# Optimization experiments

Hardware: AMD Instinct MI355X
Metric: run time of the kernel (lower is better)

Reference implementation:

```python
import jax, jax.numpy as jnp
import numpy as np

B, N, D_MODEL, H = 2, 2048, 1024, 16
HD = D_MODEL // H  # head_dim = 64

def setup_inputs() -> dict:
    key = jax.random.key(0)
    ks = jax.random.split(key, 5)
    x = jax.random.normal(ks[0], (B, N, D_MODEL), dtype=jnp.float32)
    scale = 0.02
    # Linear weights stored as [in, out] (torch does x @ W.T with W [out,in]; equivalent math)
    Wq = jax.random.normal(ks[1], (D_MODEL, D_MODEL), dtype=jnp.float32) * scale
    Wk = jax.random.normal(ks[2], (D_MODEL, D_MODEL), dtype=jnp.float32) * scale
    Wv = jax.random.normal(ks[3], (D_MODEL, D_MODEL), dtype=jnp.float32) * scale
    Wo = jax.random.normal(ks[4], (D_MODEL, D_MODEL), dtype=jnp.float32) * scale
    return {"x": x, "Wq": Wq, "Wk": Wk, "Wv": Wv, "Wo": Wo}

def reference(x, Wq, Wk, Wv, Wo):
    b, n, _ = x.shape
    # QKV projections (no bias; qkv_bias=False)
    q = (x @ Wq).reshape(b, n, H, HD)
    k = (x @ Wk).reshape(b, n, H, HD)
    v = (x @ Wv).reshape(b, n, H, HD)
    # scores [b, h, q, k]
    scores = jnp.einsum('bqhd,bkhd->bhqk', q, k) / jnp.sqrt(jnp.float32(HD))
    causal = jnp.triu(jnp.ones((n, n), dtype=bool), k=1)  # True above diagonal -> masked
    scores = jnp.where(causal, -jnp.inf, scores)
    attn = jax.nn.softmax(scores, axis=-1)  # dropout p=0.0 -> identity
    ctx = jnp.einsum('bhqk,bkhd->bqhd', attn, v).reshape(b, n, D_MODEL)
    return ctx @ Wo
```

## Files before the change

### kernel.cpp

```cpp
#include <hip/hip_runtime.h>
#include <math.h>

#define D_MODEL 1024
#define NHEAD 16
#define HD 64
#define SEQ 2048
#define BATCH 2
#define MTOT (BATCH * SEQ)

typedef __attribute__((ext_vector_type(8))) short bf16x8;
typedef __attribute__((ext_vector_type(4))) float f32x4;

__device__ __forceinline__ unsigned short f2bf(float f) {
    unsigned int u = __float_as_uint(f);
    u += 0x7FFF + ((u >> 16) & 1);
    return (unsigned short)(u >> 16);
}

__device__ __forceinline__ unsigned int pk2bf(float a, float b) {
    unsigned int r;
    asm("v_cvt_pk_bf16_f32 %0, %1, %2" : "=v"(r) : "v"(a), "v"(b));
    return r;
}

__device__ __forceinline__ void async16(unsigned short* lds, const unsigned short* g) {
    __builtin_amdgcn_global_load_lds(
        (const __attribute__((address_space(1))) unsigned int*)g,
        (__attribute__((address_space(3))) unsigned int*)lds, 16, 0, 0);
}

__device__ __forceinline__ void BAR() {
    asm volatile("" ::: "memory");
    __builtin_amdgcn_s_barrier();
    asm volatile("" ::: "memory");
}

__global__ __launch_bounds__(256) void prep(const float* __restrict__ x,
                                            unsigned short* __restrict__ xb,
                                            const float* __restrict__ W0,
                                            const float* __restrict__ W1,
                                            const float* __restrict__ W2,
                                            const float* __restrict__ W3,
                                            unsigned short* __restrict__ Wt) {
    const int bid = blockIdx.x;
    const int tid = threadIdx.x;
    if (bid < 4096) {
        const int i = (bid * 256 + tid) * 4;
        float4 v = *(const float4*)(x + i);
        uint2 pk;
        pk.x = pk2bf(v.x, v.y);
        pk.y = pk2bf(v.z, v.w);
        *(uint2*)(xb + i) = pk;
    } else {
        __shared__ float T[32][33];
        const int t = bid - 4096;
        const int z = t >> 10, rem = t & 1023;
        const int n0 = (rem & 31) * 32, k0 = (rem >> 5) * 32;
        const float* W = (z == 0) ? W0 : (z == 1) ? W1 : (z == 2) ? W2 : W3;
        unsigned short* out = Wt + (size_t)z * D_MODEL * D_MODEL;
        const int tx = tid & 31, ty = tid >> 5;
#pragma unroll
        for (int i = 0; i < 4; ++i)
            T[ty + 8 * i][tx] = W[(size_t)(k0 + ty + 8 * i) * D_MODEL + n0 + tx];
        __syncthreads();
#pragma unroll
        for (int i = 0; i < 4; ++i)
            out[(size_t)(n0 + ty + 8 * i) * D_MODEL + k0 + tx] = f2bf(T[tx][ty + 8 * i]);
    }
}

__global__ __launch_bounds__(512, 2) void qkv_mfma(const unsigned short* __restrict__ A,
                                                   const unsigned short* __restrict__ Wt,
                                                   unsigned short* __restrict__ q,
                                                   unsigned short* __restrict__ k,
                                                   unsigned short* __restrict__ vt) {
    __shared__ unsigned short SM[40960];
    const int tid = threadIdx.x;
    const int wave = tid >> 6, lane = tid & 63;
    const int quad = lane >> 4, l16 = lane & 15;
    const int wm = wave >> 2, wn = wave & 3;

    const int bid = blockIdx.x;
    const int swz = (bid & 7) * 64 + (bid >> 3);
    const int by = swz >> 4, bx = swz & 15;
    const int m0 = by * 128;
    const int c0 = bx * 192;
    const unsigned short* Bz = Wt;

    const unsigned short* aptr;
    {
        const int s = tid, r = s >> 2;
        const int cg = (s & 3) ^ ((r + (r >> 2)) & 3);
        aptr = A + (size_t)(m0 + r) * D_MODEL + cg * 8;
    }
    const unsigned short* bptr[2];
#pragma unroll
    for (int j = 0; j < 2; ++j) {
        const int s = j * 512 + tid;
        const int r = s >> 2;
        const int cg = (s & 3) ^ ((r + (r >> 2)) & 3);
        const int rb = (r < 192) ? r : 191;
        bptr[j] = Bz + (size_t)(c0 + rb) * D_MODEL + cg * 8;
    }
    const int ldsA0 = wave * 512;
    const int ldsB0 = wave * 512, ldsB1 = 4096 + wave * 512;

    const int key = (l16 + (l16 >> 2)) & 3;
    const int chunk = quad ^ key;
    int aoff[4], boff[3];
#pragma unroll
    for (int mt = 0; mt < 4; ++mt)
        aoff[mt] = ((wm * 64 + mt * 16 + l16) * 4 + chunk) * 8;
#pragma unroll
    for (int nt = 0; nt < 3; ++nt)
        boff[nt] = ((wn * 48 + nt * 16 + l16) * 4 + chunk) * 8;

    f32x4 acc[4][3];
#pragma unroll
    for (int mt = 0; mt < 4; ++mt)
#pragma unroll
        for (int nt = 0; nt < 3; ++nt)
            acc[mt][nt] = (f32x4){0.f, 0.f, 0.f, 0.f};

    auto stageA = [&](int d, int ks, int T) {
        const int base = d * 20480 + ks * 4096;
        async16(SM + base + ldsA0, aptr + T * 64 + ks * 32);
    };
    auto stageB = [&](int d, int ks, int T) {
        const int base = d * 20480 + 8192 + ks * 6144;
        async16(SM + base + ldsB0, bptr[0] + T * 64 + ks * 32);
        if (wave < 4)
            async16(SM + base + ldsB1, bptr[1] + T * 64 + ks * 32);
    };
    auto dsA = [&](bf16x8* af, int mh, int d, int ks) {
        const int base = d * 20480 + ks * 4096;
#pragma unroll
        for (int i = 0; i < 2; ++i)
            af[i] = *(const bf16x8*)&SM[base + aoff[mh * 2 + i]];
    };
    auto dsB = [&](bf16x8* bf, int d, int ks) {
        const int base = d * 20480 + 8192 + ks * 6144;
#pragma unroll
        for (int i = 0; i < 3; ++i)
            bf[i] = *(const bf16x8*)&SM[base + boff[i]];
    };
    auto mfma6 = [&](bf16x8* af, bf16x8* bf, int mh) {
        __builtin_amdgcn_s_setprio(1);
#pragma unroll
        for (int i = 0; i < 2; ++i)
#pragma unroll
            for (int nt = 0; nt < 3; ++nt)
                acc[mh * 2 + i][nt] = __builtin_amdgcn_mfma_f32_16x16x32_bf16(
                    af[i], bf[nt], acc[mh * 2 + i][nt], 0, 0, 0);
        __builtin_amdgcn_s_setprio(0);
    };
    auto waitc = [&](bool nx) {
        if (nx) {
            if (wave < 4) asm volatile("s_waitcnt vmcnt(3)" ::: "memory");
            else          asm volatile("s_waitcnt vmcnt(2)" ::: "memory");
        } else {
            asm volatile("s_waitcnt vmcnt(0)" ::: "memory");
        }
    };

    stageA(0, 0, 0);
    stageB(0, 0, 0);
    stageA(0, 1, 0);
    stageB(0, 1, 0);
    waitc(true);
    BAR();

    const int NT = D_MODEL / 64;
    for (int T = 0; T < NT; ++T) {
        const int d = T & 1, dn = d ^ 1;
        const bool nx = (T + 1 < NT);
        bf16x8 af[2], bf[3];
        dsA(af, 0, d, 0);
        dsB(bf, d, 0);
        if (nx) stageA(dn, 0, T + 1);
        __builtin_amdgcn_sched_barrier(0);
        BAR();
        mfma6(af, bf, 0);
        BAR();
        dsA(af, 1, d, 0);
        if (nx) stageB(dn, 0, T + 1);
        waitc(nx);
        __builtin_amdgcn_sched_barrier(0);
        BAR();
        mfma6(af, bf, 1);
        BAR();
        dsA(af, 0, d, 1);
        dsB(bf, d, 1);
        if (nx) stageA(dn, 1, T + 1);
        __builtin_amdgcn_sched_barrier(0);
        BAR();
        mfma6(af, bf, 0);
        BAR();
        dsA(af, 1, d, 1);
        if (nx) stageB(dn, 1, T + 1);
        waitc(nx);
        __builtin_amdgcn_sched_barrier(0);
        BAR();
        mfma6(af, bf, 1);
        BAR();
    }

    __syncthreads();
    const int bb = m0 >> 11, tok0 = m0 & (SEQ - 1);
#pragma unroll 1
    for (int G = 0; G < 3; ++G) {
        if (G) __syncthreads();
        const int gcol = c0 + G * 64;
        const int zg = gcol >> 10;
        const int hg = (gcol >> 6) & 15;
        if (zg < 2) {
            const float sc = (zg == 0) ? 0.18033688011112042f : 1.0f;
            unsigned short* dst = (zg == 0) ? q : k;
#pragma unroll
            for (int nt = 0; nt < 3; ++nt) {
                const int colb = wn * 48 + nt * 16;
                if ((colb >> 6) == G) {
                    const int cl = colb - G * 64 + l16;
#pragma unroll
                    for (int mt = 0; mt < 4; ++mt)
#pragma unroll
                        for (int reg = 0; reg < 4; ++reg) {
                            const int rr = wm * 64 + mt * 16 + quad * 4 + reg;
                            SM[rr * 64 + cl] = f2bf(acc[mt][nt][reg] * sc);
                        }
                }
            }
            __syncthreads();
#pragma unroll
            for (int it = 0; it < 2; ++it) {
                const int g = it * 512 + tid;
                const int r = g >> 3, c8 = g & 7;
                uint4 val = *(const uint4*)&SM[r * 64 + c8 * 8];
                *(uint4*)(dst + (((size_t)bb * NHEAD + hg) * SEQ + tok0 + r) * HD +
                          c8 * 8) = val;
            }
        } else {
#pragma unroll
            for (int nt = 0; nt < 3; ++nt) {
                const int colb = wn * 48 + nt * 16;
                if ((colb >> 6) == G) {
                    const int dl = colb - G * 64 + l16;
#pragma unroll
                    for (int mt = 0; mt < 4; ++mt) {
                        const int m = wm * 64 + mt * 16 + quad * 4;
                        uint2 w;
                        w.x = pk2bf(acc[mt][nt][0], acc[mt][nt][1]);
                        w.y = pk2bf(acc[mt][nt][2], acc[mt][nt][3]);
                        *(uint2*)&SM[dl * 136 + m] = w;
                    }
                }
            }
            __syncthreads();
#pragma unroll
            for (int it = 0; it < 2; ++it) {
                const int g = it * 512 + tid;
                const int dd = g >> 4, t8 = (g & 15) * 8;
                uint4 val = *(const uint4*)&SM[dd * 136 + t8];
                *(uint4*)(vt + (((size_t)bb * NHEAD + hg) * HD + dd) * SEQ + tok0 +
                          t8) = val;
            }
        }
    }
}

__global__ __launch_bounds__(256) void gemm_out(const unsigned short* __restrict__ A,
                                                const unsigned short* __restrict__ Bw,
                                                float* __restrict__ outf) {
    __shared__ unsigned short SM[12288];
    const int tid = threadIdx.x;
    const int m0 = blockIdx.y * 64, n0 = blockIdx.x * 128;
    const int wave = tid >> 6, lane = tid & 63;
    const int quad = lane >> 4, l16 = lane & 15;
    const int wm = wave & 1, wn = wave >> 1;

    f32x4 acc[2][4];
#pragma unroll
    for (int mt = 0; mt < 2; ++mt)
#pragma unroll
        for (int nt = 0; nt < 4; ++nt)
            acc[mt][nt] = (f32x4){0.f, 0.f, 0.f, 0.f};

    for (int k0 = 0; k0 < D_MODEL; k0 += 64) {
        __syncthreads();
#pragma unroll
        for (int i = 0; i < 2; ++i) {
            const int c = i * 256 + tid;
            const int r = c >> 3, cc = (c & 7) * 8;
            const int cbase = i * 256 + wave * 64;
            async16(SM + cbase * 8, A + (size_t)(m0 + r) * D_MODEL + k0 + cc);
        }
#pragma unroll
        for (int i = 0; i < 4; ++i) {
            const int c = i * 256 + tid;
            const int r = c >> 3, cc = (c & 7) * 8;
            const int cbase = i * 256 + wave * 64;
            async16(SM + 4096 + cbase * 8, Bw + (size_t)(n0 + r) * D_MODEL + k0 + cc);
        }
        __syncthreads();
#pragma unroll
        for (int ks = 0; ks < 2; ++ks) {
            bf16x8 af[2], bfr[4];
#pragma unroll
            for (int mt = 0; mt < 2; ++mt)
                af[mt] = *(const bf16x8*)&SM[(wm * 32 + mt * 16 + l16) * 64 + ks * 32 + quad * 8];
#pragma unroll
            for (int nt = 0; nt < 4; ++nt)
                bfr[nt] = *(const bf16x8*)&SM[4096 + (wn * 64 + nt * 16 + l16) * 64 + ks * 32 + quad * 8];
#pragma unroll
            for (int mt = 0; mt < 2; ++mt)
#pragma unroll
                for (int nt = 0; nt < 4; ++nt)
                    acc[mt][nt] = __builtin_amdgcn_mfma_f32_16x16x32_bf16(
                        af[mt], bfr[nt], acc[mt][nt], 0, 0, 0);
        }
    }

#pragma unroll
    for (int mt = 0; mt < 2; ++mt)
#pragma unroll
        for (int nt = 0; nt < 4; ++nt)
#pragma unroll
            for (int reg = 0; reg < 4; ++reg) {
                const int m = m0 + wm * 32 + mt * 16 + quad * 4 + reg;
                const int n = n0 + wn * 64 + nt * 16 + l16;
                outf[(size_t)m * D_MODEL + n] = acc[mt][nt][reg];
            }
}

__global__ __launch_bounds__(256, 2) void attn_mfma(const unsigned short* __restrict__ Q,
                                                    const unsigned short* __restrict__ K,
                                                    const unsigned short* __restrict__ VT,
                                                    unsigned short* __restrict__ ctx) {
    __shared__ float CMB[8832];
    const int tid = threadIdx.x;
    const int wave = tid >> 6, lane = tid & 63;
    const int quad = lane >> 4, l16 = lane & 15;
    const int h = blockIdx.x, b = blockIdx.z;
    const int y = blockIdx.y;
    const unsigned short* Qp = Q + ((size_t)b * NHEAD + h) * SEQ * HD;
    const unsigned short* Kp = K + ((size_t)b * NHEAD + h) * SEQ * HD;
    const unsigned short* Vp = VT + ((size_t)b * NHEAD + h) * HD * SEQ;
    unsigned short* Pw = (unsigned short*)CMB + wave * 4096;
    const int sw8 = l16 & 7;

#pragma unroll 1
    for (int half = 0; half < 2; ++half) {
        const int p = half ? y : (31 - y);
        const int row0 = p * 64;
        if (half) __syncthreads();

        bf16x8 bQ[4][2];
#pragma unroll
        for (int f = 0; f < 4; ++f)
#pragma unroll
            for (int ks = 0; ks < 2; ++ks)
                bQ[f][ks] = *(const bf16x8*)(Qp +
                    (size_t)(row0 + f * 16 + l16) * HD + ks * 32 + quad * 8);

        f32x4 o[4][4];
        float ps[4] = {0.f, 0.f, 0.f, 0.f};
#pragma unroll
        for (int nt = 0; nt < 4; ++nt)
#pragma unroll
            for (int f = 0; f < 4; ++f)
                o[nt][f] = (f32x4){0.f, 0.f, 0.f, 0.f};

        for (int kt = wave; kt <= p; kt += 4) {
            bf16x8 aK[4][2];
#pragma unroll
            for (int mt = 0; mt < 4; ++mt)
#pragma unroll
                for (int ks = 0; ks < 2; ++ks)
                    aK[mt][ks] = *(const bf16x8*)(Kp +
                        (size_t)(kt * 64 + mt * 16 + l16) * HD + ks * 32 + quad * 8);

            f32x4 sT[4][4];
            __builtin_amdgcn_s_setprio(1);
#pragma unroll
            for (int mt = 0; mt < 4; ++mt)
#pragma unroll
                for (int f = 0; f < 4; ++f) {
                    sT[mt][f] = __builtin_amdgcn_mfma_f32_16x16x32_bf16(
                        aK[mt][0], bQ[f][0], (f32x4){0.f, 0.f, 0.f, 0.f}, 0, 0, 0);
                    sT[mt][f] = __builtin_amdgcn_mfma_f32_16x16x32_bf16(
                        aK[mt][1], bQ[f][1], sT[mt][f], 0, 0, 0);
                }
            __builtin_amdgcn_s_setprio(0);

            bf16x8 aV[4][2];
#pragma unroll
            for (int nt = 0; nt < 4; ++nt)
#pragma unroll
                for (int ks = 0; ks < 2; ++ks)
                    aV[nt][ks] = *(const bf16x8*)(Vp +
                        (size_t)(nt * 16 + l16) * SEQ + kt * 64 + ks * 32 + quad * 8);

            const bool diag = (kt == p);
#pragma unroll
            for (int mt = 0; mt < 4; ++mt)
#pragma unroll
                for (int f = 0; f < 4; ++f) {
                    float pv[4];
#pragma unroll
                    for (int reg = 0; reg < 4; ++reg)
                        pv[reg] = __builtin_amdgcn_exp2f(sT[mt][f][reg]);
                    if (diag) {
                        const int kb = kt * 64 + mt * 16 + quad * 4;
                        const int qg = row0 + f * 16 + l16;
#pragma unroll
                        for (int reg = 0; reg < 4; ++reg)
                            pv[reg] = (kb + reg > qg) ? 0.f : pv[reg];
                    }
                    ps[f] += (pv[0] + pv[1]) + (pv[2] + pv[3]);
                    uint2 w;
                    w.x = pk2bf(pv[0], pv[1]);
                    w.y = pk2bf(pv[2], pv[3]);
                    const int gph = ((mt * 2 + (quad >> 1)) ^ sw8);
                    *(uint2*)&Pw[(f * 16 + l16) * 64 + gph * 8 + (quad & 1) * 4] = w;
                }

            bf16x8 bP[4][2];
#pragma unroll
            for (int f = 0; f < 4; ++f)
#pragma unroll
                for (int ks = 0; ks < 2; ++ks)
                    bP[f][ks] = *(const bf16x8*)&Pw[(f * 16 + l16) * 64 +
                                                    ((ks * 4 + quad) ^ sw8) * 8];

            __builtin_amdgcn_s_setprio(1);
#pragma unroll
            for (int nt = 0; nt < 4; ++nt)
#pragma unroll
                for (int f = 0; f < 4; ++f) {
                    o[nt][f] = __builtin_amdgcn_mfma_f32_16x16x32_bf16(
                        aV[nt][0], bP[f][0], o[nt][f], 0, 0, 0);
                    o[nt][f] = __builtin_amdgcn_mfma_f32_16x16x32_bf16(
                        aV[nt][1], bP[f][1], o[nt][f], 0, 0, 0);
                }
            __builtin_amdgcn_s_setprio(0);
        }

#pragma unroll
        for (int f = 0; f < 4; ++f) {
            ps[f] += __shfl_xor(ps[f], 16);
            ps[f] += __shfl_xor(ps[f], 32);
        }

        __syncthreads();
        if (wave >= 2) {
            float* Rg = CMB + (wave - 2) * 4352;
#pragma unroll
            for (int nt = 0; nt < 4; ++nt)
#pragma unroll
                for (int f = 0; f < 4; ++f)
                    *(f32x4*)&Rg[(f * 16 + l16) * 68 + nt * 16 + quad * 4] = o[nt][f];
            if (quad == 0)
#pragma unroll
                for (int f = 0; f < 4; ++f)
                    CMB[8704 + (wave - 2) * 64 + f * 16 + l16] = ps[f];
        }
        __syncthreads();
        if (wave < 2) {
            float* Rg = CMB + wave * 4352;
#pragma unroll
            for (int nt = 0; nt < 4; ++nt)
#pragma unroll
                for (int f = 0; f < 4; ++f)
                    o[nt][f] += *(const f32x4*)&Rg[(f * 16 + l16) * 68 + nt * 16 + quad * 4];
#pragma unroll
            for (int f = 0; f < 4; ++f)
                ps[f] += CMB[8704 + wave * 64 + f * 16 + l16];
        }
        __syncthreads();
        if (wave == 1) {
#pragma unroll
            for (int nt = 0; nt < 4; ++nt)
#pragma unroll
                for (int f = 0; f < 4; ++f)
                    *(f32x4*)&CMB[(f * 16 + l16) * 68 + nt * 16 + quad * 4] = o[nt][f];
            if (quad == 0)
#pragma unroll
                for (int f = 0; f < 4; ++f)
                    CMB[8704 + f * 16 + l16] = ps[f];
        }
        __syncthreads();
        if (wave == 0) {
#pragma unroll
            for (int nt = 0; nt < 4; ++nt)
#pragma unroll
                for (int f = 0; f < 4; ++f)
                    o[nt][f] += *(const f32x4*)&CMB[(f * 16 + l16) * 68 + nt * 16 + quad * 4];
            float inv[4];
#pragma unroll
            for (int f = 0; f < 4; ++f)
                inv[f] = 1.f / (ps[f] + CMB[8704 + f * 16 + l16]);
#pragma unroll
            for (int nt = 0; nt < 4; ++nt)
#pragma unroll
                for (int f = 0; f < 4; ++f) {
                    const int tok = row0 + f * 16 + l16;
                    const int col = h * HD + nt * 16 + quad * 4;
                    uint2 w;
                    w.x = pk2bf(o[nt][f][0] * inv[f], o[nt][f][1] * inv[f]);
                    w.y = pk2bf(o[nt][f][2] * inv[f], o[nt][f][3] * inv[f]);
                    *(uint2*)(ctx + ((size_t)b * SEQ + tok) * D_MODEL + col) = w;
                }
        }
    }
}

extern "C" void kernel_launch(void* const* d_in, const int* in_sizes, int n_in,
                              void* d_out, int out_size, void* d_ws, size_t ws_size,
                              hipStream_t stream) {
    const float* x  = (const float*)d_in[0];
    const float* Wq = (const float*)d_in[1];
    const float* Wk = (const float*)d_in[2];
    const float* Wv = (const float*)d_in[3];
    const float* Wo = (const float*)d_in[4];
    float* out = (float*)d_out;

    unsigned short* ws = (unsigned short*)d_ws;
    const size_t T = (size_t)MTOT * D_MODEL;
    unsigned short* xb  = ws;
    unsigned short* Wt  = ws + T;
    unsigned short* q   = ws + 2 * T;
    unsigned short* k   = ws + 3 * T;
    unsigned short* vt  = ws + 4 * T;
    unsigned short* ctx = ws + 5 * T;

    prep<<<dim3(8192), dim3(256), 0, stream>>>(x, xb, Wq, Wk, Wv, Wo, Wt);

    qkv_mfma<<<dim3(512), dim3(512), 0, stream>>>(xb, Wt, q, k, vt);

    attn_mfma<<<dim3(NHEAD, 16, BATCH), dim3(256), 0, stream>>>(q, k, vt, ctx);

    gemm_out<<<dim3(8, 64), dim3(256), 0, stream>>>(ctx, Wt + 3 * (size_t)D_MODEL * D_MODEL, out);
}
```

Before: 174.2 us.

## Restructure attention: split query rows across waves, double-buffer K/V in LDS

```diff
diff --git a/kernel.cpp b/kernel.cpp
--- a/kernel.cpp
+++ b/kernel.cpp
@@ -332,185 +332,143 @@
             }
 }
 
-__global__ __launch_bounds__(256, 2) void attn_mfma(const unsigned short* __restrict__ Q,
+__global__ __launch_bounds__(256, 4) void attn_mfma(const unsigned short* __restrict__ Q,
                                                     const unsigned short* __restrict__ K,
                                                     const unsigned short* __restrict__ VT,
                                                     unsigned short* __restrict__ ctx) {
-    __shared__ float CMB[8832];
+    __shared__ unsigned short SM[20480];
     const int tid = threadIdx.x;
     const int wave = tid >> 6, lane = tid & 63;
     const int quad = lane >> 4, l16 = lane & 15;
     const int h = blockIdx.x, b = blockIdx.z;
-    const int y = blockIdx.y;
+    const int p = 31 - (int)blockIdx.y;
+    const int row0 = p * 64;
+    const int qrow = row0 + wave * 16 + l16;
     const unsigned short* Qp = Q + ((size_t)b * NHEAD + h) * SEQ * HD;
     const unsigned short* Kp = K + ((size_t)b * NHEAD + h) * SEQ * HD;
     const unsigned short* Vp = VT + ((size_t)b * NHEAD + h) * HD * SEQ;
-    unsigned short* Pw = (unsigned short*)CMB + wave * 4096;
+    unsigned short* Pw = SM + 16384 + wave * 1024;
     const int sw8 = l16 & 7;
 
-#pragma unroll 1
-    for (int half = 0; half < 2; ++half) {
-        const int p = half ? y : (31 - y);
-        const int row0 = p * 64;
-        if (half) __syncthreads();
-
-        bf16x8 bQ[4][2];
-#pragma unroll
-        for (int f = 0; f < 4; ++f)
+    const unsigned short* kptr[2];
+    const unsigned short* vptr[2];
+    int ldsoff[2];
+#pragma unroll
+    for (int j = 0; j < 2; ++j) {
+        const int c = j * 256 + tid;
+        const int r = c >> 3, s = c & 7;
+        const int sg = (s ^ (r & 7)) * 8;
+        kptr[j] = Kp + (size_t)r * HD + sg;
+        vptr[j] = Vp + (size_t)r * SEQ + sg;
+        ldsoff[j] = (j * 256 + wave * 64) * 8;
+    }
+    auto stageKV = [&](int d, int kt) {
+        const int kb = d * 4096, vb = 8192 + d * 4096;
+#pragma unroll
+        for (int j = 0; j < 2; ++j) {
+            async16(SM + kb + ldsoff[j], kptr[j] + (size_t)kt * 64 * HD);
+            async16(SM + vb + ldsoff[j], vptr[j] + kt * 64);
+        }
+    };
+
+    bf16x8 bQ[2];
+#pragma unroll
+    for (int ks = 0; ks < 2; ++ks)
+        bQ[ks] = *(const bf16x8*)(Qp + (size_t)qrow * HD + ks * 32 + quad * 8);
+
+    f32x4 o[4];
+    float ps = 0.f;
+#pragma unroll
+    for (int nt = 0; nt < 4; ++nt)
+        o[nt] = (f32x4){0.f, 0.f, 0.f, 0.f};
+
+    stageKV(0, 0);
+    asm volatile("s_waitcnt vmcnt(0)" ::: "memory");
+    BAR();
+
+    for (int kt = 0; kt <= p; ++kt) {
+        const int cur = kt & 1;
+        const int kbase = cur * 4096, vbase = 8192 + cur * 4096;
+
+        bf16x8 aK[4][2];
+#pragma unroll
+        for (int mt = 0; mt < 4; ++mt)
 #pragma unroll
             for (int ks = 0; ks < 2; ++ks)
-                bQ[f][ks] = *(const bf16x8*)(Qp +
-                    (size_t)(row0 + f * 16 + l16) * HD + ks * 32 + quad * 8);
-
-        f32x4 o[4][4];
-        float ps[4] = {0.f, 0.f, 0.f, 0.f};
+                aK[mt][ks] = *(const bf16x8*)&SM[kbase + (mt * 16 + l16) * 64 +
+                                                 (((ks * 4 + quad)) ^ sw8) * 8];
+
+        if (kt < p) stageKV(cur ^ 1, kt + 1);
+
+        f32x4 sT[4];
+        __builtin_amdgcn_s_setprio(1);
+#pragma unroll
+        for (int mt = 0; mt < 4; ++mt) {
+            sT[mt] = __builtin_amdgcn_mfma_f32_16x16x32_bf16(
+                aK[mt][0], bQ[0], (f32x4){0.f, 0.f, 0.f, 0.f}, 0, 0, 0);
+            sT[mt] = __builtin_amdgcn_mfma_f32_16x16x32_bf16(
+                aK[mt][1], bQ[1], sT[mt], 0, 0, 0);
+        }
+        __builtin_amdgcn_s_setprio(0);
+
+        const bool diag = (kt == p);
+#pragma unroll
+        for (int mt = 0; mt < 4; ++mt) {
+            float pv[4];
+#pragma unroll
+            for (int reg = 0; reg < 4; ++reg)
+                pv[reg] = __builtin_amdgcn_exp2f(sT[mt][reg]);
+            if (diag) {
+                const int kb = kt * 64 + mt * 16 + quad * 4;
+#pragma unroll
+                for (int reg = 0; reg < 4; ++reg)
+                    pv[reg] = (kb + reg > qrow) ? 0.f : pv[reg];
+            }
+            ps += (pv[0] + pv[1]) + (pv[2] + pv[3]);
+            uint2 w;
+            w.x = pk2bf(pv[0], pv[1]);
+            w.y = pk2bf(pv[2], pv[3]);
+            const int gph = ((mt * 2 + (quad >> 1)) ^ sw8);
+            *(uint2*)&Pw[l16 * 64 + gph * 8 + (quad & 1) * 4] = w;
+        }
+
+        bf16x8 bP[2];
+#pragma unroll
+        for (int ks = 0; ks < 2; ++ks)
+            bP[ks] = *(const bf16x8*)&Pw[l16 * 64 + ((ks * 4 + quad) ^ sw8) * 8];
+
+        bf16x8 aV[4][2];
 #pragma unroll
         for (int nt = 0; nt < 4; ++nt)
 #pragma unroll
-            for (int f = 0; f < 4; ++f)
-                o[nt][f] = (f32x4){0.f, 0.f, 0.f, 0.f};
-
-        for (int kt = wave; kt <= p; kt += 4) {
-            bf16x8 aK[4][2];
-#pragma unroll
-            for (int mt = 0; mt < 4; ++mt)
-#pragma unroll
-                for (int ks = 0; ks < 2; ++ks)
-                    aK[mt][ks] = *(const bf16x8*)(Kp +
-                        (size_t)(kt * 64 + mt * 16 + l16) * HD + ks * 32 + quad * 8);
-
-            f32x4 sT[4][4];
-            __builtin_amdgcn_s_setprio(1);
-#pragma unroll
-            for (int mt = 0; mt < 4; ++mt)
-#pragma unroll
-                for (int f = 0; f < 4; ++f) {
-                    sT[mt][f] = __builtin_amdgcn_mfma_f32_16x16x32_bf16(
-                        aK[mt][0], bQ[f][0], (f32x4){0.f, 0.f, 0.f, 0.f}, 0, 0, 0);
-                    sT[mt][f] = __builtin_amdgcn_mfma_f32_16x16x32_bf16(
-                        aK[mt][1], bQ[f][1], sT[mt][f], 0, 0, 0);
-                }
-            __builtin_amdgcn_s_setprio(0);
-
-            bf16x8 aV[4][2];
-#pragma unroll
-            for (int nt = 0; nt < 4; ++nt)
-#pragma unroll
-                for (int ks = 0; ks < 2; ++ks)
-                    aV[nt][ks] = *(const bf16x8*)(Vp +
-                        (size_t)(nt * 16 + l16) * SEQ + kt * 64 + ks * 32 + quad * 8);
-
-            const bool diag = (kt == p);
-#pragma unroll
-            for (int mt = 0; mt < 4; ++mt)
-#pragma unroll
-                for (int f = 0; f < 4; ++f) {
-                    float pv[4];
-#pragma unroll
-                    for (int reg = 0; reg < 4; ++reg)
-                        pv[reg] = __builtin_amdgcn_exp2f(sT[mt][f][reg]);
-                    if (diag) {
-                        const int kb = kt * 64 + mt * 16 + quad * 4;
-                        const int qg = row0 + f * 16 + l16;
-#pragma unroll
-                        for (int reg = 0; reg < 4; ++reg)
-                            pv[reg] = (kb + reg > qg) ? 0.f : pv[reg];
-                    }
-                    ps[f] += (pv[0] + pv[1]) + (pv[2] + pv[3]);
-                    uint2 w;
-                    w.x = pk2bf(pv[0], pv[1]);
-                    w.y = pk2bf(pv[2], pv[3]);
-                    const int gph = ((mt * 2 + (quad >> 1)) ^ sw8);
-                    *(uint2*)&Pw[(f * 16 + l16) * 64 + gph * 8 + (quad & 1) * 4] = w;
-                }
-
-            bf16x8 bP[4][2];
-#pragma unroll
-            for (int f = 0; f < 4; ++f)
-#pragma unroll
-                for (int ks = 0; ks < 2; ++ks)
-                    bP[f][ks] = *(const bf16x8*)&Pw[(f * 16 + l16) * 64 +
-                                                    ((ks * 4 + quad) ^ sw8) * 8];
-
-            __builtin_amdgcn_s_setprio(1);
-#pragma unroll
-            for (int nt = 0; nt < 4; ++nt)
-#pragma unroll
-                for (int f = 0; f < 4; ++f) {
-                    o[nt][f] = __builtin_amdgcn_mfma_f32_16x16x32_bf16(
-                        aV[nt][0], bP[f][0], o[nt][f], 0, 0, 0);
-                    o[nt][f] = __builtin_amdgcn_mfma_f32_16x16x32_bf16(
-                        aV[nt][1], bP[f][1], o[nt][f], 0, 0, 0);
-                }
-            __builtin_amdgcn_s_setprio(0);
-        }
-
-#pragma unroll
-        for (int f = 0; f < 4; ++f) {
-            ps[f] += __shfl_xor(ps[f], 16);
-            ps[f] += __shfl_xor(ps[f], 32);
-        }
-
-        __syncthreads();
-        if (wave >= 2) {
-            float* Rg = CMB + (wave - 2) * 4352;
-#pragma unroll
-            for (int nt = 0; nt < 4; ++nt)
-#pragma unroll
-                for (int f = 0; f < 4; ++f)
-                    *(f32x4*)&Rg[(f * 16 + l16) * 68 + nt * 16 + quad * 4] = o[nt][f];
-            if (quad == 0)
-#pragma unroll
-                for (int f = 0; f < 4; ++f)
-                    CMB[8704 + (wave - 2) * 64 + f * 16 + l16] = ps[f];
-        }
-        __syncthreads();
-        if (wave < 2) {
-            float* Rg = CMB + wave * 4352;
-#pragma unroll
-            for (int nt = 0; nt < 4; ++nt)
-#pragma unroll
-                for (int f = 0; f < 4; ++f)
-                    o[nt][f] += *(const f32x4*)&Rg[(f * 16 + l16) * 68 + nt * 16 + quad * 4];
-#pragma unroll
-            for (int f = 0; f < 4; ++f)
-                ps[f] += CMB[8704 + wave * 64 + f * 16 + l16];
-        }
-        __syncthreads();
-        if (wave == 1) {
-#pragma unroll
-            for (int nt = 0; nt < 4; ++nt)
-#pragma unroll
-                for (int f = 0; f < 4; ++f)
-                    *(f32x4*)&CMB[(f * 16 + l16) * 68 + nt * 16 + quad * 4] = o[nt][f];
-            if (quad == 0)
-#pragma unroll
-                for (int f = 0; f < 4; ++f)
-                    CMB[8704 + f * 16 + l16] = ps[f];
-        }
-        __syncthreads();
-        if (wave == 0) {
-#pragma unroll
-            for (int nt = 0; nt < 4; ++nt)
-#pragma unroll
-                for (int f = 0; f < 4; ++f)
-                    o[nt][f] += *(const f32x4*)&CMB[(f * 16 + l16) * 68 + nt * 16 + quad * 4];
-            float inv[4];
-#pragma unroll
-            for (int f = 0; f < 4; ++f)
-                inv[f] = 1.f / (ps[f] + CMB[8704 + f * 16 + l16]);
-#pragma unroll
-            for (int nt = 0; nt < 4; ++nt)
-#pragma unroll
-                for (int f = 0; f < 4; ++f) {
-                    const int tok = row0 + f * 16 + l16;
-                    const int col = h * HD + nt * 16 + quad * 4;
-                    uint2 w;
-                    w.x = pk2bf(o[nt][f][0] * inv[f], o[nt][f][1] * inv[f]);
-                    w.y = pk2bf(o[nt][f][2] * inv[f], o[nt][f][3] * inv[f]);
-                    *(uint2*)(ctx + ((size_t)b * SEQ + tok) * D_MODEL + col) = w;
-                }
-        }
+            for (int ks = 0; ks < 2; ++ks)
+                aV[nt][ks] = *(const bf16x8*)&SM[vbase + (nt * 16 + l16) * 64 +
+                                                 (((ks * 4 + quad)) ^ sw8) * 8];
+        __builtin_amdgcn_s_setprio(1);
+#pragma unroll
+        for (int nt = 0; nt < 4; ++nt) {
+            o[nt] = __builtin_amdgcn_mfma_f32_16x16x32_bf16(
+                aV[nt][0], bP[0], o[nt], 0, 0, 0);
+            o[nt] = __builtin_amdgcn_mfma_f32_16x16x32_bf16(
+                aV[nt][1], bP[1], o[nt], 0, 0, 0);
+        }
+        __builtin_amdgcn_s_setprio(0);
+
+        asm volatile("s_waitcnt vmcnt(0)" ::: "memory");
+        BAR();
+    }
+
+    ps += __shfl_xor(ps, 16);
+    ps += __shfl_xor(ps, 32);
+    const float inv = 1.f / ps;
+
+#pragma unroll
+    for (int nt = 0; nt < 4; ++nt) {
+        const int col = h * HD + nt * 16 + quad * 4;
+        uint2 w;
+        w.x = pk2bf(o[nt][0] * inv, o[nt][1] * inv);
+        w.y = pk2bf(o[nt][2] * inv, o[nt][3] * inv);
+        *(uint2*)(ctx + ((size_t)b * SEQ + qrow) * D_MODEL + col) = w;
     }
 }
 
@@ -537,7 +495,7 @@
 
     qkv_mfma<<<dim3(512), dim3(512), 0, stream>>>(xb, Wt, q, k, vt);
 
-    attn_mfma<<<dim3(NHEAD, 16, BATCH), dim3(256), 0, stream>>>(q, k, vt, ctx);
+    attn_mfma<<<dim3(NHEAD, 32, BATCH), dim3(256), 0, stream>>>(q, k, vt, ctx);
 
     gemm_out<<<dim3(8, 64), dim3(256), 0, stream>>>(ctx, Wt + 3 * (size_t)D_MODEL * D_MODEL, out);
 }
```

After: 170.0 us. 2.5% less time.
